# Performance work log

Hardware: AMD Instinct MI355X
Metric: run time of the kernel (lower is better)

The kernel has to match this reference:

```python
import jax, jax.numpy as jnp
import numpy as np

B, L, D, Y = 8, 2048, 512, 8921


def setup_inputs() -> dict:
    key = jax.random.key(0)
    k1, k2, k3, k4, k5 = jax.random.split(key, 5)
    x = jax.random.normal(k1, (B, L, D), dtype=jnp.float32)
    target = (jax.random.uniform(k2, (B, Y), dtype=jnp.float32) < 0.01).astype(jnp.float32)
    text_inputs = jnp.zeros((B, L), dtype=jnp.int64)
    # xavier-uniform-ish init for the two [Y, D] weight matrices
    bound = float(np.sqrt(6.0 / (Y + D)))
    U_weight = jax.random.uniform(k3, (Y, D), minval=-bound, maxval=bound, dtype=jnp.float32)
    final_weight = jax.random.uniform(k4, (Y, D), minval=-bound, maxval=bound, dtype=jnp.float32)
    final_bias = jax.random.normal(k5, (Y,), dtype=jnp.float32) * 0.01
    return {"x": x, "target": target, "text_inputs": text_inputs,
            "U_weight": U_weight, "final_weight": final_weight, "final_bias": final_bias}


def reference(x, target, text_inputs, U_weight, final_weight, final_bias):
    # alpha = softmax(U.weight @ x^T, dim=seq)  -> [B, Y, L]
    scores = jnp.einsum('yd,bld->byl', U_weight, x)
    alpha = jax.nn.softmax(scores, axis=-1)
    # m = alpha @ x  -> [B, Y, D]
    m = jnp.einsum('byl,bld->byd', alpha, x)
    # y = sum(final.weight * m, dim=-1) + final.bias  -> [B, Y]
    y = jnp.sum(final_weight * m, axis=-1) + final_bias
    # BCEWithLogitsLoss (mean reduction), numerically stable form
    loss = jnp.mean(jnp.maximum(y, 0.0) - y * target + jnp.log1p(jnp.exp(-jnp.abs(y))))
    return (y, loss, alpha, m)
```

## Files before the change

kernel.cpp:

```cpp
#include <hip/hip_runtime.h>
#include <hip/hip_bf16.h>

#define B_ 8
#define L_ 2048
#define D_ 512
#define Y_ 8921

typedef __bf16 bf16;
typedef __attribute__((ext_vector_type(8))) __bf16 bf16x8;
typedef __attribute__((ext_vector_type(4))) __bf16 bf16x4;
typedef __attribute__((ext_vector_type(4))) float f32x4;

#define MFMA16(a,b,c) __builtin_amdgcn_mfma_f32_16x16x32_bf16((a),(b),(c),0,0,0)

#define OFF_LOSS  71368ull
#define OFF_ALPHA 71369ull
#define OFF_M     146233033ull

#define WS_XB 0ull
#define WS_XT 16777216ull
#define WS_UB 33554432ull
#define WS_AB 42689536ull

#define GLOAD_LDS16(gsrc, ldst) \
  __builtin_amdgcn_global_load_lds((const __attribute__((address_space(1))) void*)(gsrc), \
                                   (__attribute__((address_space(3))) void*)(ldst), 16, 0, 0)

__global__ void prep_x_kernel(const float* __restrict__ x, bf16* __restrict__ xb,
                              bf16* __restrict__ xT)
{
  __shared__ bf16 tile[64][65];
  const int b = blockIdx.z, l0 = blockIdx.x * 64, d0 = blockIdx.y * 64;
  const int t = threadIdx.x;
  const int r = t >> 4, c4 = (t & 15) * 4;
  const float* xp = x + ((size_t)b * L_ + l0) * D_ + d0;
  #pragma unroll
  for (int i = 0; i < 4; i++) {
    int rr = r + i * 16;
    float4 v = *(const float4*)(xp + (size_t)rr * D_ + c4);
    bf16 b0 = (bf16)v.x, b1 = (bf16)v.y, b2 = (bf16)v.z, b3 = (bf16)v.w;
    bf16x4 pk = {b0, b1, b2, b3};
    *(bf16x4*)(xb + ((size_t)b * L_ + l0 + rr) * D_ + d0 + c4) = pk;
    tile[rr][c4 + 0] = b0; tile[rr][c4 + 1] = b1;
    tile[rr][c4 + 2] = b2; tile[rr][c4 + 3] = b3;
  }
  __syncthreads();
  #pragma unroll
  for (int i = 0; i < 4; i++) {
    int dd = r + i * 16;
    bf16x4 pk = {tile[c4 + 0][dd], tile[c4 + 1][dd], tile[c4 + 2][dd], tile[c4 + 3][dd]};
    *(bf16x4*)(xT + ((size_t)b * D_ + d0 + dd) * L_ + l0 + c4) = pk;
  }
}

__global__ void prep_u_kernel(const float* __restrict__ U, bf16* __restrict__ Ub)
{
  size_t i4 = ((size_t)blockIdx.x * 256 + threadIdx.x) * 4;
  if (i4 >= (size_t)Y_ * D_) return;
  float4 v = *(const float4*)(U + i4);
  bf16x4 pk = {(bf16)v.x, (bf16)v.y, (bf16)v.z, (bf16)v.w};
  *(bf16x4*)(Ub + i4) = pk;
}

__global__ __launch_bounds__(512, 2) void k1_scores_softmax(
    const bf16* __restrict__ xb, const bf16* __restrict__ Ub,
    float* __restrict__ alphaF, bf16* __restrict__ alphaB)
{
  const int b = blockIdx.y;
  const int y0 = blockIdx.x * 32;
  const int tid = threadIdx.x;
  const int w = tid >> 6, lane = tid & 63;
  const int r15 = lane & 15, koct = lane >> 4;

  const bf16* xB = xb + (size_t)b * (L_ * D_);
  f32x4 acc[2][16];
  #pragma unroll
  for (int mt = 0; mt < 2; mt++)
    #pragma unroll
    for (int nt = 0; nt < 16; nt++) acc[mt][nt] = (f32x4){0.f, 0.f, 0.f, 0.f};

  int yy0 = y0 + r15;      if (yy0 > Y_ - 1) yy0 = Y_ - 1;
  int yy1 = y0 + 16 + r15; if (yy1 > Y_ - 1) yy1 = Y_ - 1;
  const bf16* ap0 = Ub + (size_t)yy0 * D_ + koct * 8;
  const bf16* ap1 = Ub + (size_t)yy1 * D_ + koct * 8;
  const bf16* bp  = xB + (size_t)(w * 256 + r15) * D_ + koct * 8;

  for (int k0 = 0; k0 < D_; k0 += 32) {
    bf16x8 a0 = *(const bf16x8*)(ap0 + k0);
    bf16x8 a1 = *(const bf16x8*)(ap1 + k0);
    #pragma unroll
    for (int nt = 0; nt < 16; nt++) {
      bf16x8 bb = *(const bf16x8*)(bp + (size_t)nt * (16 * D_) + k0);
      acc[0][nt] = MFMA16(a0, bb, acc[0][nt]);
      acc[1][nt] = MFMA16(a1, bb, acc[1][nt]);
    }
  }

  __shared__ float red[8][32];
  __shared__ float rowstat[32];

  float rmax[2][4];
  #pragma unroll
  for (int mt = 0; mt < 2; mt++)
    #pragma unroll
    for (int q = 0; q < 4; q++) {
      float m = acc[mt][0][q];
      #pragma unroll
      for (int nt = 1; nt < 16; nt++) m = fmaxf(m, acc[mt][nt][q]);
      #pragma unroll
      for (int off = 1; off < 16; off <<= 1) m = fmaxf(m, __shfl_xor(m, off, 64));
      rmax[mt][q] = m;
    }
  if (r15 == 0) {
    #pragma unroll
    for (int mt = 0; mt < 2; mt++)
      #pragma unroll
      for (int q = 0; q < 4; q++) red[w][mt * 16 + koct * 4 + q] = rmax[mt][q];
  }
  __syncthreads();
  if (tid < 32) {
    float m = red[0][tid];
    #pragma unroll
    for (int ww = 1; ww < 8; ww++) m = fmaxf(m, red[ww][tid]);
    rowstat[tid] = m;
  }
  __syncthreads();

  #pragma unroll
  for (int mt = 0; mt < 2; mt++)
    #pragma unroll
    for (int q = 0; q < 4; q++) {
      float mx = rowstat[mt * 16 + koct * 4 + q];
      float s = 0.f;
      #pragma unroll
      for (int nt = 0; nt < 16; nt++) {
        float p = __expf(acc[mt][nt][q] - mx);
        acc[mt][nt][q] = p;
        s += p;
      }
      #pragma unroll
      for (int off = 1; off < 16; off <<= 1) s += __shfl_xor(s, off, 64);
      if (r15 == 0) red[w][mt * 16 + koct * 4 + q] = s;
    }
  __syncthreads();
  if (tid < 32) {
    float s = 0.f;
    #pragma unroll
    for (int ww = 0; ww < 8; ww++) s += red[ww][tid];
    rowstat[tid] = 1.0f / s;
  }
  __syncthreads();

  #pragma unroll
  for (int mt = 0; mt < 2; mt++) {
    #pragma unroll
    for (int q = 0; q < 4; q++) {
      int row = mt * 16 + koct * 4 + q;
      int yg = y0 + row;
      if (yg >= Y_) continue;
      float inv = rowstat[row];
      float* dstF = alphaF + ((size_t)b * Y_ + yg) * L_ + w * 256 + r15;
      bf16*  dstB = alphaB + ((size_t)b * Y_ + yg) * L_ + w * 256 + r15;
      #pragma unroll
      for (int nt = 0; nt < 16; nt++) {
        float aV = acc[mt][nt][q] * inv;
        dstF[nt * 16] = aV;
        dstB[nt * 16] = (bf16)aV;
      }
    }
  }
}

__global__ __launch_bounds__(512, 2) void k2_m_y_loss(
    const bf16* __restrict__ alphaB, const bf16* __restrict__ xT,
    const float* __restrict__ FW, const float* __restrict__ bias,
    const float* __restrict__ target, float* __restrict__ out)
{
  const int b = blockIdx.y;
  const int y0 = blockIdx.x * 128;
  const int tid = threadIdx.x;
  const int w = tid >> 6, lane = tid & 63;
  const int r15 = lane & 15, koct = lane >> 4;

  __shared__ bf16 At[2][128 * 64];

  f32x4 acc[8][4];
  #pragma unroll
  for (int mt = 0; mt < 8; mt++)
    #pragma unroll
    for (int nt = 0; nt < 4; nt++) acc[mt][nt] = (f32x4){0.f, 0.f, 0.f, 0.f};

  auto stage = [&](int kk, int bufI) {
    #pragma unroll
    for (int rd = 0; rd < 2; rd++) {
      int r = rd * 64 + w * 8 + (lane >> 3);
      int sg = (lane & 7) ^ (lane >> 3);
      int yg = y0 + r; if (yg > Y_ - 1) yg = Y_ - 1;
      const bf16* src = alphaB + ((size_t)b * Y_ + yg) * L_ + kk * 64 + sg * 8;
      GLOAD_LDS16(src, &At[bufI][rd * 4096 + w * 512]);
    }
  };

  const bf16* bp = xT + ((size_t)b * D_ + w * 64 + r15) * L_ + koct * 8;

  stage(0, 0);
  for (int kk = 0; kk < 32; kk++) {
    __syncthreads();
    if (kk + 1 < 32) stage(kk + 1, (kk + 1) & 1);
    const bf16* At_cur = &At[kk & 1][0];
    const int k0 = kk * 64;
    #pragma unroll
    for (int kh = 0; kh < 2; kh++) {
      bf16x8 bfr[4];
      #pragma unroll
      for (int nt = 0; nt < 4; nt++)
        bfr[nt] = *(const bf16x8*)(bp + (size_t)nt * (16 * L_) + k0 + kh * 32);
      #pragma unroll
      for (int mt = 0; mt < 8; mt++) {
        int r = mt * 16 + r15;
        int slot = (kh * 4 + koct) ^ (r & 7);
        bf16x8 afr = *(const bf16x8*)(At_cur + r * 64 + slot * 8);
        #pragma unroll
        for (int nt = 0; nt < 4; nt++) acc[mt][nt] = MFMA16(afr, bfr[nt], acc[mt][nt]);
      }
    }
  }

  float ypart[8][4];
  #pragma unroll
  for (int mt = 0; mt < 8; mt++) {
    #pragma unroll
    for (int q = 0; q < 4; q++) {
      int row = mt * 16 + koct * 4 + q;
      int yg = y0 + row;
      bool ok = (yg < Y_);
      int ygc = ok ? yg : (Y_ - 1);
      const float* fw = FW + (size_t)ygc * D_ + w * 64 + r15;
      float* mrow = out + OFF_M + ((size_t)b * Y_ + ygc) * D_ + w * 64 + r15;
      float p = 0.f;
      #pragma unroll
      for (int nt = 0; nt < 4; nt++) {
        float v = acc[mt][nt][q];
        if (ok) mrow[nt * 16] = v;
        p += v * fw[nt * 16];
      }
      ypart[mt][q] = p;
    }
  }
  #pragma unroll
  for (int mt = 0; mt < 8; mt++)
    #pragma unroll
    for (int q = 0; q < 4; q++) {
      float p = ypart[mt][q];
      #pragma unroll
      for (int off = 1; off < 16; off <<= 1) p += __shfl_xor(p, off, 64);
      ypart[mt][q] = p;
    }
  __shared__ float yred[8][128];
  if (r15 == 0) {
    #pragma unroll
    for (int mt = 0; mt < 8; mt++)
      #pragma unroll
      for (int q = 0; q < 4; q++) yred[w][mt * 16 + koct * 4 + q] = ypart[mt][q];
  }
  __syncthreads();
  if (tid < 128) {
    int yg = y0 + tid;
    float s = 0.f;
    #pragma unroll
    for (int ww = 0; ww < 8; ww++) s += yred[ww][tid];
    float lterm = 0.f;
    if (yg < Y_) {
      float yv = s + bias[yg];
      out[(size_t)b * Y_ + yg] = yv;
      float tv = target[(size_t)b * Y_ + yg];
      lterm = fmaxf(yv, 0.f) - yv * tv + log1pf(__expf(-fabsf(yv)));
    }
    #pragma unroll
    for (int off = 1; off < 64; off <<= 1) lterm += __shfl_xor(lterm, off, 64);
    if ((tid & 63) == 0)
      atomicAdd(out + OFF_LOSS, lterm * (1.0f / ((float)B_ * (float)Y_)));
  }
}

extern "C" void kernel_launch(void* const* d_in, const int* in_sizes, int n_in,
                              void* d_out, int out_size, void* d_ws, size_t ws_size,
                              hipStream_t stream) {
  const float* x      = (const float*)d_in[0];
  const float* target = (const float*)d_in[1];
  const float* U      = (const float*)d_in[3];
  const float* FW     = (const float*)d_in[4];
  const float* bias   = (const float*)d_in[5];
  float* out = (float*)d_out;

  char* ws = (char*)d_ws;
  bf16* xb = (bf16*)(ws + WS_XB);
  bf16* xT = (bf16*)(ws + WS_XT);
  bf16* Ub = (bf16*)(ws + WS_UB);
  bf16* aB = (bf16*)(ws + WS_AB);

  hipMemsetAsync((char*)d_out + OFF_LOSS * 4, 0, 4, stream);

  prep_x_kernel<<<dim3(L_ / 64, D_ / 64, B_), 256, 0, stream>>>(x, xb, xT);
  prep_u_kernel<<<dim3((Y_ * D_ / 4 + 255) / 256), 256, 0, stream>>>(U, Ub);

  k1_scores_softmax<<<dim3((Y_ + 31) / 32, B_), 512, 0, stream>>>(
      xb, Ub, out + OFF_ALPHA, aB);

  k2_m_y_loss<<<dim3((Y_ + 127) / 128, B_), 512, 0, stream>>>(
      aB, xT, FW, bias, target, out);
}
```

Before: 1.874 ms.

## Split softmax into tiled partial-max GEMM with rescale, deferring alpha write to m GEMM

The scores GEMM now runs on 128x128 LDS-staged tiles over (y, l) and produces unnormalized exp values with per-tile row max and sum. A small kernel combines these into per-tile scale factors. The m GEMM applies the scales while staging, writes the fp32 alpha output from there, and is split over two halves of D, and a final kernel computes y and the loss. This aims to improve operand reuse and occupancy over the previous register-only k1, at the cost of an extra bf16 P buffer, more launches, and rereading P in both D halves.

```diff
diff --git a/kernel.cpp b/kernel.cpp
--- a/kernel.cpp
+++ b/kernel.cpp
@@ -5,6 +5,8 @@
 #define L_ 2048
 #define D_ 512
 #define Y_ 8921
+#define YPAD 8960
+#define NLT 16
 
 typedef __bf16 bf16;
 typedef __attribute__((ext_vector_type(8))) __bf16 bf16x8;
@@ -20,7 +22,11 @@
 #define WS_XB 0ull
 #define WS_XT 16777216ull
 #define WS_UB 33554432ull
-#define WS_AB 42689536ull
+#define WS_P  42729472ull
+#define WS_PM 336330752ull
+#define WS_PS 340918272ull
+#define WS_SC 345505792ull
+#define WS_YP 350093312ull
 
 #define GLOAD_LDS16(gsrc, ldst) \
   __builtin_amdgcn_global_load_lds((const __attribute__((address_space(1))) void*)(gsrc), \
@@ -56,187 +62,235 @@
 __global__ void prep_u_kernel(const float* __restrict__ U, bf16* __restrict__ Ub)
 {
   size_t i4 = ((size_t)blockIdx.x * 256 + threadIdx.x) * 4;
-  if (i4 >= (size_t)Y_ * D_) return;
-  float4 v = *(const float4*)(U + i4);
+  if (i4 >= (size_t)YPAD * D_) return;
+  int r = (int)(i4 >> 9);
+  int c = (int)(i4 & 511);
+  int rs = r < Y_ ? r : (Y_ - 1);
+  float4 v = *(const float4*)(U + (size_t)rs * D_ + c);
   bf16x4 pk = {(bf16)v.x, (bf16)v.y, (bf16)v.z, (bf16)v.w};
   *(bf16x4*)(Ub + i4) = pk;
 }
 
-__global__ __launch_bounds__(512, 2) void k1_scores_softmax(
+__global__ __launch_bounds__(512, 4) void k1_gemm_pexp(
     const bf16* __restrict__ xb, const bf16* __restrict__ Ub,
-    float* __restrict__ alphaF, bf16* __restrict__ alphaB)
-{
-  const int b = blockIdx.y;
-  const int y0 = blockIdx.x * 32;
+    bf16* __restrict__ P, float* __restrict__ pmax, float* __restrict__ psum)
+{
+  const int yt = blockIdx.x, lt = blockIdx.y, b = blockIdx.z;
+  const int y0 = yt * 128, l0 = lt * 128;
   const int tid = threadIdx.x;
   const int w = tid >> 6, lane = tid & 63;
+  const int wr = w >> 2, wc = w & 3;
   const int r15 = lane & 15, koct = lane >> 4;
 
+  __shared__ bf16 As[2][128 * 64];
+  __shared__ bf16 Bs[2][128 * 64];
+  __shared__ float redm[2][64][4];
+  __shared__ float reds[2][64][4];
+
+  f32x4 acc[4][2];
+  #pragma unroll
+  for (int mt = 0; mt < 4; mt++)
+    #pragma unroll
+    for (int nt = 0; nt < 2; nt++) acc[mt][nt] = (f32x4){0.f, 0.f, 0.f, 0.f};
+
   const bf16* xB = xb + (size_t)b * (L_ * D_);
-  f32x4 acc[2][16];
-  #pragma unroll
-  for (int mt = 0; mt < 2; mt++)
-    #pragma unroll
-    for (int nt = 0; nt < 16; nt++) acc[mt][nt] = (f32x4){0.f, 0.f, 0.f, 0.f};
-
-  int yy0 = y0 + r15;      if (yy0 > Y_ - 1) yy0 = Y_ - 1;
-  int yy1 = y0 + 16 + r15; if (yy1 > Y_ - 1) yy1 = Y_ - 1;
-  const bf16* ap0 = Ub + (size_t)yy0 * D_ + koct * 8;
-  const bf16* ap1 = Ub + (size_t)yy1 * D_ + koct * 8;
-  const bf16* bp  = xB + (size_t)(w * 256 + r15) * D_ + koct * 8;
-
-  for (int k0 = 0; k0 < D_; k0 += 32) {
-    bf16x8 a0 = *(const bf16x8*)(ap0 + k0);
-    bf16x8 a1 = *(const bf16x8*)(ap1 + k0);
-    #pragma unroll
-    for (int nt = 0; nt < 16; nt++) {
-      bf16x8 bb = *(const bf16x8*)(bp + (size_t)nt * (16 * D_) + k0);
-      acc[0][nt] = MFMA16(a0, bb, acc[0][nt]);
-      acc[1][nt] = MFMA16(a1, bb, acc[1][nt]);
-    }
-  }
-
-  __shared__ float red[8][32];
-  __shared__ float rowstat[32];
-
-  float rmax[2][4];
-  #pragma unroll
-  for (int mt = 0; mt < 2; mt++)
+  const int srow = (lane >> 3), scol = (lane & 7) * 8;
+
+  auto stage = [&](int kk, int bufI) {
+    #pragma unroll
+    for (int i = 0; i < 2; i++) {
+      int c = w * 2 + i;
+      int row = c * 8 + srow;
+      GLOAD_LDS16(Ub + (size_t)(y0 + row) * D_ + kk * 64 + scol, &As[bufI][c * 512]);
+      GLOAD_LDS16(xB + (size_t)(l0 + row) * D_ + kk * 64 + scol, &Bs[bufI][c * 512]);
+    }
+  };
+
+  stage(0, 0);
+  for (int kk = 0; kk < 8; kk++) {
+    __syncthreads();
+    if (kk < 7) stage(kk + 1, (kk + 1) & 1);
+    const bf16* Ac = As[kk & 1];
+    const bf16* Bc = Bs[kk & 1];
+    #pragma unroll
+    for (int kh = 0; kh < 2; kh++) {
+      bf16x8 af[4], bfr[2];
+      #pragma unroll
+      for (int mt = 0; mt < 4; mt++)
+        af[mt] = *(const bf16x8*)(Ac + (wr * 64 + mt * 16 + r15) * 64 + kh * 32 + koct * 8);
+      #pragma unroll
+      for (int nt = 0; nt < 2; nt++)
+        bfr[nt] = *(const bf16x8*)(Bc + (wc * 32 + nt * 16 + r15) * 64 + kh * 32 + koct * 8);
+      #pragma unroll
+      for (int mt = 0; mt < 4; mt++)
+        #pragma unroll
+        for (int nt = 0; nt < 2; nt++)
+          acc[mt][nt] = MFMA16(af[mt], bfr[nt], acc[mt][nt]);
+    }
+  }
+
+  #pragma unroll
+  for (int mt = 0; mt < 4; mt++)
     #pragma unroll
     for (int q = 0; q < 4; q++) {
-      float m = acc[mt][0][q];
-      #pragma unroll
-      for (int nt = 1; nt < 16; nt++) m = fmaxf(m, acc[mt][nt][q]);
+      float m = fmaxf(acc[mt][0][q], acc[mt][1][q]);
       #pragma unroll
       for (int off = 1; off < 16; off <<= 1) m = fmaxf(m, __shfl_xor(m, off, 64));
-      rmax[mt][q] = m;
-    }
-  if (r15 == 0) {
-    #pragma unroll
-    for (int mt = 0; mt < 2; mt++)
-      #pragma unroll
-      for (int q = 0; q < 4; q++) red[w][mt * 16 + koct * 4 + q] = rmax[mt][q];
-  }
-  __syncthreads();
-  if (tid < 32) {
-    float m = red[0][tid];
-    #pragma unroll
-    for (int ww = 1; ww < 8; ww++) m = fmaxf(m, red[ww][tid]);
-    rowstat[tid] = m;
-  }
-  __syncthreads();
-
-  #pragma unroll
-  for (int mt = 0; mt < 2; mt++)
+      if (r15 == 0) redm[wr][mt * 16 + koct * 4 + q][wc] = m;
+    }
+  __syncthreads();
+  #pragma unroll
+  for (int mt = 0; mt < 4; mt++)
     #pragma unroll
     for (int q = 0; q < 4; q++) {
-      float mx = rowstat[mt * 16 + koct * 4 + q];
+      int r64 = mt * 16 + koct * 4 + q;
+      float M4 = fmaxf(fmaxf(redm[wr][r64][0], redm[wr][r64][1]),
+                       fmaxf(redm[wr][r64][2], redm[wr][r64][3]));
+      int grow = y0 + wr * 64 + r64;
+      bf16* dst = P + ((size_t)b * YPAD + grow) * L_ + l0 + wc * 32 + r15;
       float s = 0.f;
       #pragma unroll
-      for (int nt = 0; nt < 16; nt++) {
-        float p = __expf(acc[mt][nt][q] - mx);
-        acc[mt][nt][q] = p;
+      for (int nt = 0; nt < 2; nt++) {
+        float p = __expf(acc[mt][nt][q] - M4);
+        dst[nt * 16] = (bf16)p;
         s += p;
       }
       #pragma unroll
       for (int off = 1; off < 16; off <<= 1) s += __shfl_xor(s, off, 64);
-      if (r15 == 0) red[w][mt * 16 + koct * 4 + q] = s;
-    }
-  __syncthreads();
-  if (tid < 32) {
-    float s = 0.f;
-    #pragma unroll
-    for (int ww = 0; ww < 8; ww++) s += red[ww][tid];
-    rowstat[tid] = 1.0f / s;
-  }
-  __syncthreads();
-
-  #pragma unroll
-  for (int mt = 0; mt < 2; mt++) {
-    #pragma unroll
-    for (int q = 0; q < 4; q++) {
-      int row = mt * 16 + koct * 4 + q;
-      int yg = y0 + row;
-      if (yg >= Y_) continue;
-      float inv = rowstat[row];
-      float* dstF = alphaF + ((size_t)b * Y_ + yg) * L_ + w * 256 + r15;
-      bf16*  dstB = alphaB + ((size_t)b * Y_ + yg) * L_ + w * 256 + r15;
-      #pragma unroll
-      for (int nt = 0; nt < 16; nt++) {
-        float aV = acc[mt][nt][q] * inv;
-        dstF[nt * 16] = aV;
-        dstB[nt * 16] = (bf16)aV;
-      }
-    }
-  }
-}
-
-__global__ __launch_bounds__(512, 2) void k2_m_y_loss(
-    const bf16* __restrict__ alphaB, const bf16* __restrict__ xT,
-    const float* __restrict__ FW, const float* __restrict__ bias,
-    const float* __restrict__ target, float* __restrict__ out)
+      if (r15 == 0) reds[wr][r64][wc] = s;
+    }
+  __syncthreads();
+  if (tid < 128) {
+    int wr2 = tid >> 6, r64 = tid & 63;
+    float M = fmaxf(fmaxf(redm[wr2][r64][0], redm[wr2][r64][1]),
+                    fmaxf(redm[wr2][r64][2], redm[wr2][r64][3]));
+    float S = reds[wr2][r64][0] + reds[wr2][r64][1] + reds[wr2][r64][2] + reds[wr2][r64][3];
+    size_t idx = ((size_t)b * NLT + lt) * YPAD + y0 + tid;
+    pmax[idx] = M;
+    psum[idx] = S;
+  }
+}
+
+__global__ void k1b_scale(const float* __restrict__ pmax, const float* __restrict__ psum,
+                          float* __restrict__ scale)
 {
   const int b = blockIdx.y;
-  const int y0 = blockIdx.x * 128;
+  const int y = blockIdx.x * 256 + threadIdx.x;
+  float pm[NLT];
+  float M = -1e30f;
+  #pragma unroll
+  for (int lt = 0; lt < NLT; lt++) {
+    pm[lt] = pmax[((size_t)b * NLT + lt) * YPAD + y];
+    M = fmaxf(M, pm[lt]);
+  }
+  float S = 0.f;
+  #pragma unroll
+  for (int lt = 0; lt < NLT; lt++)
+    S += psum[((size_t)b * NLT + lt) * YPAD + y] * __expf(pm[lt] - M);
+  float inv = 1.0f / S;
+  #pragma unroll
+  for (int lt = 0; lt < NLT; lt++)
+    scale[((size_t)b * NLT + lt) * YPAD + y] = __expf(pm[lt] - M) * inv;
+}
+
+__global__ __launch_bounds__(512, 4) void k2_m_y(
+    const bf16* __restrict__ P, const bf16* __restrict__ xT,
+    const float* __restrict__ scale, const float* __restrict__ FW,
+    float* __restrict__ out, float* __restrict__ yp)
+{
+  const int yt = blockIdx.x, dh = blockIdx.y, b = blockIdx.z;
+  const int y0 = yt * 128, d0 = dh * 256;
   const int tid = threadIdx.x;
   const int w = tid >> 6, lane = tid & 63;
+  const int wr = w >> 2, wc = w & 3;
   const int r15 = lane & 15, koct = lane >> 4;
 
-  __shared__ bf16 At[2][128 * 64];
-
-  f32x4 acc[8][4];
-  #pragma unroll
-  for (int mt = 0; mt < 8; mt++)
+  __shared__ bf16 As[2][128 * 32];
+  __shared__ bf16 Bs[2][256 * 32];
+  __shared__ float scl[NLT * 128];
+  __shared__ float yred[128][4];
+
+  for (int i = tid; i < NLT * 128; i += 512) {
+    int lt2 = i >> 7, r = i & 127;
+    scl[i] = scale[((size_t)b * NLT + lt2) * YPAD + y0 + r];
+  }
+
+  f32x4 acc[4][4];
+  #pragma unroll
+  for (int mt = 0; mt < 4; mt++)
     #pragma unroll
     for (int nt = 0; nt < 4; nt++) acc[mt][nt] = (f32x4){0.f, 0.f, 0.f, 0.f};
 
-  auto stage = [&](int kk, int bufI) {
-    #pragma unroll
-    for (int rd = 0; rd < 2; rd++) {
-      int r = rd * 64 + w * 8 + (lane >> 3);
-      int sg = (lane & 7) ^ (lane >> 3);
-      int yg = y0 + r; if (yg > Y_ - 1) yg = Y_ - 1;
-      const bf16* src = alphaB + ((size_t)b * Y_ + yg) * L_ + kk * 64 + sg * 8;
-      GLOAD_LDS16(src, &At[bufI][rd * 4096 + w * 512]);
-    }
+  const int ar = tid >> 2, akc = (tid & 3) * 8;
+  const bf16* aps = P + ((size_t)b * YPAD + y0 + ar) * L_ + akc;
+  float* afs = out + OFF_ALPHA + ((size_t)b * Y_ + y0 + ar) * (size_t)L_ + akc;
+  const bool awrite = (dh == 0) && (y0 + ar < Y_);
+
+  auto writeA = [&](int kk, int bufI, bf16x8 pv) {
+    float s = scl[(kk >> 2) * 128 + ar];
+    float a[8];
+    #pragma unroll
+    for (int j = 0; j < 8; j++) a[j] = (float)pv[j] * s;
+    if (awrite) {
+      #pragma unroll
+      for (int j = 0; j < 8; j++) afs[(size_t)kk * 32 + j] = a[j];
+    }
+    bf16x8 ab;
+    #pragma unroll
+    for (int j = 0; j < 8; j++) ab[j] = (bf16)a[j];
+    *(bf16x8*)(&As[bufI][ar * 32 + akc]) = ab;
   };
-
-  const bf16* bp = xT + ((size_t)b * D_ + w * 64 + r15) * L_ + koct * 8;
-
-  stage(0, 0);
-  for (int kk = 0; kk < 32; kk++) {
+  const int brow = (lane >> 2), bcol = (lane & 3) * 8;
+  auto stageB = [&](int kk, int bufI) {
+    #pragma unroll
+    for (int i = 0; i < 2; i++) {
+      int c = w * 2 + i;
+      int row = c * 16 + brow;
+      GLOAD_LDS16(xT + ((size_t)b * D_ + d0 + row) * L_ + kk * 32 + bcol, &Bs[bufI][c * 512]);
+    }
+  };
+
+  __syncthreads();
+  {
+    bf16x8 pv0 = *(const bf16x8*)(aps);
+    stageB(0, 0);
+    writeA(0, 0, pv0);
+  }
+
+  for (int kk = 0; kk < 64; kk++) {
     __syncthreads();
-    if (kk + 1 < 32) stage(kk + 1, (kk + 1) & 1);
-    const bf16* At_cur = &At[kk & 1][0];
-    const int k0 = kk * 64;
-    #pragma unroll
-    for (int kh = 0; kh < 2; kh++) {
-      bf16x8 bfr[4];
+    bf16x8 pv;
+    if (kk < 63) {
+      pv = *(const bf16x8*)(aps + (size_t)(kk + 1) * 32);
+      stageB(kk + 1, (kk + 1) & 1);
+    }
+    const bf16* Ac = As[kk & 1];
+    const bf16* Bc = Bs[kk & 1];
+    bf16x8 af[4], bfr[4];
+    #pragma unroll
+    for (int mt = 0; mt < 4; mt++)
+      af[mt] = *(const bf16x8*)(Ac + (wr * 64 + mt * 16 + r15) * 32 + koct * 8);
+    #pragma unroll
+    for (int nt = 0; nt < 4; nt++)
+      bfr[nt] = *(const bf16x8*)(Bc + (wc * 64 + nt * 16 + r15) * 32 + koct * 8);
+    #pragma unroll
+    for (int mt = 0; mt < 4; mt++)
       #pragma unroll
       for (int nt = 0; nt < 4; nt++)
-        bfr[nt] = *(const bf16x8*)(bp + (size_t)nt * (16 * L_) + k0 + kh * 32);
-      #pragma unroll
-      for (int mt = 0; mt < 8; mt++) {
-        int r = mt * 16 + r15;
-        int slot = (kh * 4 + koct) ^ (r & 7);
-        bf16x8 afr = *(const bf16x8*)(At_cur + r * 64 + slot * 8);
-        #pragma unroll
-        for (int nt = 0; nt < 4; nt++) acc[mt][nt] = MFMA16(afr, bfr[nt], acc[mt][nt]);
-      }
-    }
-  }
-
-  float ypart[8][4];
-  #pragma unroll
-  for (int mt = 0; mt < 8; mt++) {
+        acc[mt][nt] = MFMA16(af[mt], bfr[nt], acc[mt][nt]);
+    if (kk < 63) writeA(kk + 1, (kk + 1) & 1, pv);
+  }
+
+  #pragma unroll
+  for (int mt = 0; mt < 4; mt++)
     #pragma unroll
     for (int q = 0; q < 4; q++) {
-      int row = mt * 16 + koct * 4 + q;
+      int row = wr * 64 + mt * 16 + koct * 4 + q;
       int yg = y0 + row;
       bool ok = (yg < Y_);
       int ygc = ok ? yg : (Y_ - 1);
-      const float* fw = FW + (size_t)ygc * D_ + w * 64 + r15;
-      float* mrow = out + OFF_M + ((size_t)b * Y_ + ygc) * D_ + w * 64 + r15;
+      const float* fw = FW + (size_t)ygc * D_ + d0 + wc * 64 + r15;
+      float* mrow = out + OFF_M + ((size_t)b * Y_ + ygc) * D_ + d0 + wc * 64 + r15;
       float p = 0.f;
       #pragma unroll
       for (int nt = 0; nt < 4; nt++) {
@@ -244,43 +298,37 @@
         if (ok) mrow[nt * 16] = v;
         p += v * fw[nt * 16];
       }
-      ypart[mt][q] = p;
-    }
-  }
-  #pragma unroll
-  for (int mt = 0; mt < 8; mt++)
-    #pragma unroll
-    for (int q = 0; q < 4; q++) {
-      float p = ypart[mt][q];
       #pragma unroll
       for (int off = 1; off < 16; off <<= 1) p += __shfl_xor(p, off, 64);
-      ypart[mt][q] = p;
-    }
-  __shared__ float yred[8][128];
-  if (r15 == 0) {
-    #pragma unroll
-    for (int mt = 0; mt < 8; mt++)
-      #pragma unroll
-      for (int q = 0; q < 4; q++) yred[w][mt * 16 + koct * 4 + q] = ypart[mt][q];
-  }
+      if (r15 == 0) yred[row][wc] = p;
+    }
   __syncthreads();
   if (tid < 128) {
-    int yg = y0 + tid;
-    float s = 0.f;
-    #pragma unroll
-    for (int ww = 0; ww < 8; ww++) s += yred[ww][tid];
-    float lterm = 0.f;
-    if (yg < Y_) {
-      float yv = s + bias[yg];
-      out[(size_t)b * Y_ + yg] = yv;
-      float tv = target[(size_t)b * Y_ + yg];
-      lterm = fmaxf(yv, 0.f) - yv * tv + log1pf(__expf(-fabsf(yv)));
-    }
-    #pragma unroll
-    for (int off = 1; off < 64; off <<= 1) lterm += __shfl_xor(lterm, off, 64);
-    if ((tid & 63) == 0)
-      atomicAdd(out + OFF_LOSS, lterm * (1.0f / ((float)B_ * (float)Y_)));
-  }
+    float s = yred[tid][0] + yred[tid][1] + yred[tid][2] + yred[tid][3];
+    yp[((size_t)b * 2 + dh) * YPAD + y0 + tid] = s;
+  }
+}
+
+__global__ void k3_y_loss(const float* __restrict__ yp, const float* __restrict__ bias,
+                          const float* __restrict__ target, float* __restrict__ out)
+{
+  const int b = blockIdx.y;
+  const int y = blockIdx.x * 256 + threadIdx.x;
+  float lterm = 0.f;
+  if (y < Y_) {
+    float v = yp[((size_t)b * 2) * YPAD + y] + yp[((size_t)b * 2 + 1) * YPAD + y] + bias[y];
+    out[(size_t)b * Y_ + y] = v;
+    float t = target[(size_t)b * Y_ + y];
+    lterm = fmaxf(v, 0.f) - v * t + log1pf(__expf(-fabsf(v)));
+  }
+  #pragma unroll
+  for (int off = 1; off < 64; off <<= 1) lterm += __shfl_xor(lterm, off, 64);
+  __shared__ float lred[4];
+  if ((threadIdx.x & 63) == 0) lred[threadIdx.x >> 6] = lterm;
+  __syncthreads();
+  if (threadIdx.x == 0)
+    atomicAdd(out + OFF_LOSS,
+              (lred[0] + lred[1] + lred[2] + lred[3]) * (1.0f / ((float)B_ * (float)Y_)));
 }
 
 extern "C" void kernel_launch(void* const* d_in, const int* in_sizes, int n_in,
@@ -297,16 +345,19 @@
   bf16* xb = (bf16*)(ws + WS_XB);
   bf16* xT = (bf16*)(ws + WS_XT);
   bf16* Ub = (bf16*)(ws + WS_UB);
-  bf16* aB = (bf16*)(ws + WS_AB);
+  bf16* P  = (bf16*)(ws + WS_P);
+  float* pm = (float*)(ws + WS_PM);
+  float* ps = (float*)(ws + WS_PS);
+  float* sc = (float*)(ws + WS_SC);
+  float* yp = (float*)(ws + WS_YP);
 
   hipMemsetAsync((char*)d_out + OFF_LOSS * 4, 0, 4, stream);
 
   prep_x_kernel<<<dim3(L_ / 64, D_ / 64, B_), 256, 0, stream>>>(x, xb, xT);
-  prep_u_kernel<<<dim3((Y_ * D_ / 4 + 255) / 256), 256, 0, stream>>>(U, Ub);
-
-  k1_scores_softmax<<<dim3((Y_ + 31) / 32, B_), 512, 0, stream>>>(
-      xb, Ub, out + OFF_ALPHA, aB);
-
-  k2_m_y_loss<<<dim3((Y_ + 127) / 128, B_), 512, 0, stream>>>(
-      aB, xT, FW, bias, target, out);
-}
+  prep_u_kernel<<<dim3((YPAD * D_ / 4 + 255) / 256), 256, 0, stream>>>(U, Ub);
+
+  k1_gemm_pexp<<<dim3(YPAD / 128, NLT, B_), 512, 0, stream>>>(xb, Ub, P, pm, ps);
+  k1b_scale<<<dim3(YPAD / 256, B_), 256, 0, stream>>>(pm, ps, sc);
+  k2_m_y<<<dim3(YPAD / 128, 2, B_), 512, 0, stream>>>(P, xT, sc, FW, out, yp);
+  k3_y_loss<<<dim3(YPAD / 256, B_), 256, 0, stream>>>(yp, bias, target, out);
+}
```

Measured after the change: 1.554 ms. 17.1% less time.
